# Kernel optimization log

Measured on AMD Instinct MI355X. Metric: run time of the kernel, lower is better.

Reference implementation:

```python
import jax, jax.numpy as jnp
import numpy as np

N_NODES = 50000
N_EDGES = 800000
D_IN = 128
D_H = 128
D_SIG = 16
D_OUT = 128


def _linear_params(key, fan_in, fan_out):
    kw, kb = jax.random.split(key)
    bound = 1.0 / np.sqrt(fan_in)
    w = jax.random.uniform(kw, (fan_in, fan_out), jnp.float32, -bound, bound)
    b = jax.random.uniform(kb, (fan_out,), jnp.float32, -bound, bound)
    return w, b


def setup_inputs() -> dict:
    key = jax.random.key(0)
    ks = jax.random.split(key, 7)
    x = jax.random.normal(ks[0], (N_NODES, D_IN), jnp.float32)
    edge_index = jax.random.randint(ks[1], (2, N_EDGES), 0, N_NODES, jnp.int64 if jax.config.jax_enable_x64 else jnp.int32)
    enc_w, enc_b = _linear_params(ks[2], D_IN, D_H)
    sig_w, sig_b = _linear_params(ks[3], D_H, D_SIG)
    msg_w, msg_b = _linear_params(ks[4], D_H, D_H)
    agg_w, agg_b = _linear_params(ks[5], 2 * D_H, D_H)
    dec_w, dec_b = _linear_params(ks[6], D_H, D_OUT)
    return {"x": x, "edge_index": edge_index,
            "enc_w": enc_w, "enc_b": enc_b,
            "sig_w": sig_w, "sig_b": sig_b,
            "msg_w": msg_w, "msg_b": msg_b,
            "agg_w": agg_w, "agg_b": agg_b,
            "dec_w": dec_w, "dec_b": dec_b}


def reference(x, edge_index, enc_w, enc_b, sig_w, sig_b, msg_w, msg_b, agg_w, agg_b, dec_w, dec_b):
    n = x.shape[0]
    h = x @ enc_w + enc_b                                   # [N, D_H]
    sig = h @ sig_w + sig_b                                 # [N, D_SIG]
    # F.normalize: x / max(||x||_2, eps)
    sig = sig / jnp.maximum(jnp.linalg.norm(sig, axis=-1, keepdims=True), 1e-12)
    msg = jax.nn.relu(h @ msg_w + msg_b)                    # [N, D_H]

    src, dst = edge_index[0], edge_index[1]
    # per-edge signature dot product, then segment softmax over each src node's edges
    scores = jnp.sum(sig[src] * sig[dst], axis=-1)          # [E]
    smax = jax.ops.segment_max(scores, src, num_segments=n)
    smax = jnp.where(jnp.isfinite(smax), smax, 0.0)         # empty segments -> 0
    e = jnp.exp(scores - smax[src])
    denom = jax.ops.segment_sum(e, src, num_segments=n)
    w = e / denom[src]                                      # [E]
    # weighted message aggregation; nodes with no out-edges get zeros
    comm = jax.ops.segment_sum(w[:, None] * msg[dst], src, num_segments=n)  # [N, D_H]

    combined = jax.nn.relu(jnp.concatenate([h, comm], axis=-1) @ agg_w + agg_b)
    return combined @ dec_w + dec_b
```

## Files before the change

kernel.cpp:

```cpp
#include <hip/hip_runtime.h>
#include <math.h>

#define N_NODES 50000
#define N_EDGES 800000
#define CAP 64
#define NRANGE 782
#define PCAP 1280
#define EPBA 8192
#define NBA 98

typedef __attribute__((ext_vector_type(8)))  short s16x8;
typedef __attribute__((ext_vector_type(16))) float f32x16;
typedef unsigned int u32;
typedef unsigned short u16;

union U16B { uint4 u; s16x8 s; };

__device__ __forceinline__ u32 bfr(float f) {
    u32 u = __float_as_uint(f);
    return (u + 0x7FFFu + ((u >> 16) & 1u)) >> 16;
}
__device__ __forceinline__ u32 pkbf(float a, float b) { return bfr(a) | (bfr(b) << 16); }
__device__ __forceinline__ float bf2f(u32 b) { return __uint_as_float(b << 16); }
__device__ __forceinline__ float dotpair(u32 a, u32 b) {
    return bf2f(a & 0xFFFFu) * bf2f(b & 0xFFFFu) + bf2f(a >> 16) * bf2f(b >> 16);
}

__device__ __forceinline__ uint4 buildfrag(const float* d8, int hh) {
    u32 P = pkbf(d8[0], d8[1]), Q = pkbf(d8[2], d8[3]);
    u32 R = pkbf(d8[4], d8[5]), S = pkbf(d8[6], d8[7]);
    u32 sP = (u32)__shfl_xor((int)P, 32);
    u32 sQ = (u32)__shfl_xor((int)Q, 32);
    u32 sR = (u32)__shfl_xor((int)R, 32);
    u32 sS = (u32)__shfl_xor((int)S, 32);
    uint4 f;
    f.x = hh ? sR : P;  f.y = hh ? sS : Q;
    f.z = hh ? R : sP;  f.w = hh ? S : sQ;
    return f;
}
#define BUILDF(OUT, ACC, Q, HH) do { \
    float _td[8]; \
    _Pragma("unroll") for (int _z = 0; _z < 8; ++_z) _td[_z] = (ACC)[(Q)*8 + _z]; \
    (OUT) = buildfrag(_td, HH); } while (0)
#define BUILDR(OUT, ACC, Q, HH) do { \
    float _td[8]; \
    _Pragma("unroll") for (int _z = 0; _z < 8; ++_z) _td[_z] = fmaxf((ACC)[(Q)*8 + _z], 0.f); \
    (OUT) = buildfrag(_td, HH); } while (0)

__global__ __launch_bounds__(256) void k_prep(
    const float* __restrict__ enc_w, const float* __restrict__ msg_w,
    const float* __restrict__ sig_w, const float* __restrict__ agg_w,
    const float* __restrict__ dec_w,
    uint4* __restrict__ WtE, uint4* __restrict__ WtM, uint4* __restrict__ WtD,
    uint4* __restrict__ WtA0, uint4* __restrict__ WtA1, uint4* __restrict__ WtS)
{
    int gid = blockIdx.x * 256 + threadIdx.x;
    if (gid < 10240) {
        int m = gid >> 11, r = gid & 2047;
        int col = r >> 4, s = r & 15;
        const float* W; uint4* D; int kb = 0;
        if      (m == 0) { W = enc_w; D = WtE; }
        else if (m == 1) { W = msg_w; D = WtM; }
        else if (m == 2) { W = dec_w; D = WtD; }
        else if (m == 3) { W = agg_w; D = WtA0; }
        else             { W = agg_w; D = WtA1; kb = 128; }
        float v[8];
        #pragma unroll
        for (int j = 0; j < 8; ++j) v[j] = W[(size_t)(kb + s * 8 + j) * 128 + col];
        uint4 w;
        w.x = pkbf(v[0], v[1]); w.y = pkbf(v[2], v[3]);
        w.z = pkbf(v[4], v[5]); w.w = pkbf(v[6], v[7]);
        D[col * 16 + (s ^ (col & 7))] = w;
    } else if (gid < 10752) {
        int r = gid - 10240;
        int row = r >> 4, s = r & 15;
        float v[8];
        #pragma unroll
        for (int j = 0; j < 8; ++j)
            v[j] = (row < 16) ? sig_w[(size_t)(s * 8 + j) * 16 + row] : 0.0f;
        uint4 w;
        w.x = pkbf(v[0], v[1]); w.y = pkbf(v[2], v[3]);
        w.z = pkbf(v[4], v[5]); w.w = pkbf(v[6], v[7]);
        WtS[row * 16 + (s ^ (row & 7))] = w;
    }
}

__global__ __launch_bounds__(256) void k_encode_m(
    const float* __restrict__ x,
    const uint4* __restrict__ WtE, const uint4* __restrict__ WtM,
    const uint4* __restrict__ WtS,
    const float* __restrict__ enc_b, const float* __restrict__ sig_b,
    const float* __restrict__ msg_b,
    uint4* __restrict__ h_g, u32* __restrict__ sig_bf, uint4* __restrict__ msg_g)
{
    __shared__ uint4 LB[2048];
    __shared__ uint4 LW[2048];
    __shared__ float LS[2176];

    const int t = threadIdx.x;
    const int node0 = blockIdx.x * 128;
    int nrem = N_NODES - node0; if (nrem > 128) nrem = 128;
    const int lane = t & 63, wid = t >> 6;
    const int l31 = lane & 31, hh = lane >> 5;
    const int nloc = wid * 32 + l31;
    const int sw7 = l31 & 7;

    #pragma unroll
    for (int it = 0; it < 8; ++it) {
        int idx = it * 256 + t;
        int nd = idx >> 4, s = idx & 15;
        float4 v0 = make_float4(0, 0, 0, 0), v1 = v0;
        if (nd < nrem) {
            const float4* px = (const float4*)(x + (size_t)(node0 + nd) * 128 + s * 8);
            v0 = px[0]; v1 = px[1];
        }
        uint4 w;
        w.x = pkbf(v0.x, v0.y); w.y = pkbf(v0.z, v0.w);
        w.z = pkbf(v1.x, v1.y); w.w = pkbf(v1.z, v1.w);
        LB[nd * 16 + (s ^ (nd & 7))] = w;
        LW[idx] = WtE[idx];
    }
    __syncthreads();

    const char* lb = (const char*)LB;
    const char* lw = (const char*)LW;

    f32x16 a0 = {}, a1 = {}, a2 = {}, a3 = {};
    #pragma unroll
    for (int r = 0; r < 16; ++r) {
        int rr = (r & 3) + 8 * (r >> 2) + 4 * hh;
        a0[r] = enc_b[rr];      a1[r] = enc_b[32 + rr];
        a2[r] = enc_b[64 + rr]; a3[r] = enc_b[96 + rr];
    }
    #pragma unroll
    for (int ks = 0; ks < 8; ++ks) {
        int so = ((ks * 2 + hh) ^ sw7) << 4;
        s16x8 bf = *(const s16x8*)(lb + nloc * 256 + so);
        s16x8 w0 = *(const s16x8*)(lw + l31 * 256 + so);
        s16x8 w1 = *(const s16x8*)(lw + 8192 + l31 * 256 + so);
        s16x8 w2 = *(const s16x8*)(lw + 16384 + l31 * 256 + so);
        s16x8 w3 = *(const s16x8*)(lw + 24576 + l31 * 256 + so);
        a0 = __builtin_amdgcn_mfma_f32_32x32x16_bf16(w0, bf, a0, 0, 0, 0);
        a1 = __builtin_amdgcn_mfma_f32_32x32x16_bf16(w1, bf, a1, 0, 0, 0);
        a2 = __builtin_amdgcn_mfma_f32_32x32x16_bf16(w2, bf, a2, 0, 0, 0);
        a3 = __builtin_amdgcn_mfma_f32_32x32x16_bf16(w3, bf, a3, 0, 0, 0);
    }

    uint4 hf[8];
    BUILDF(hf[0], a0, 0, hh); BUILDF(hf[1], a0, 1, hh);
    BUILDF(hf[2], a1, 0, hh); BUILDF(hf[3], a1, 1, hh);
    BUILDF(hf[4], a2, 0, hh); BUILDF(hf[5], a2, 1, hh);
    BUILDF(hf[6], a3, 0, hh); BUILDF(hf[7], a3, 1, hh);

    if (nloc < nrem) {
        const size_t rb = (size_t)(node0 + nloc) * 16;
        #pragma unroll
        for (int f = 0; f < 8; ++f) {
            int g = 2 * f + hh;
            h_g[rb + (g ^ sw7)] = hf[f];
        }
    }

    __syncthreads();
    #pragma unroll
    for (int it = 0; it < 8; ++it) LW[it * 256 + t] = WtM[it * 256 + t];
    {
        uint4* LSu = (uint4*)LS;
        LSu[t] = WtS[t]; LSu[256 + t] = WtS[256 + t];
    }
    __syncthreads();

    f32x16 m0 = {}, m1 = {}, m2 = {}, m3 = {};
    #pragma unroll
    for (int r = 0; r < 16; ++r) {
        int rr = (r & 3) + 8 * (r >> 2) + 4 * hh;
        m0[r] = msg_b[rr];      m1[r] = msg_b[32 + rr];
        m2[r] = msg_b[64 + rr]; m3[r] = msg_b[96 + rr];
    }
    #pragma unroll
    for (int ks = 0; ks < 8; ++ks) {
        int so = ((ks * 2 + hh) ^ sw7) << 4;
        U16B hb; hb.u = hf[ks];
        s16x8 w0 = *(const s16x8*)(lw + l31 * 256 + so);
        s16x8 w1 = *(const s16x8*)(lw + 8192 + l31 * 256 + so);
        s16x8 w2 = *(const s16x8*)(lw + 16384 + l31 * 256 + so);
        s16x8 w3 = *(const s16x8*)(lw + 24576 + l31 * 256 + so);
        m0 = __builtin_amdgcn_mfma_f32_32x32x16_bf16(w0, hb.s, m0, 0, 0, 0);
        m1 = __builtin_amdgcn_mfma_f32_32x32x16_bf16(w1, hb.s, m1, 0, 0, 0);
        m2 = __builtin_amdgcn_mfma_f32_32x32x16_bf16(w2, hb.s, m2, 0, 0, 0);
        m3 = __builtin_amdgcn_mfma_f32_32x32x16_bf16(w3, hb.s, m3, 0, 0, 0);
    }
    {
        uint4 mf[8];
        BUILDR(mf[0], m0, 0, hh); BUILDR(mf[1], m0, 1, hh);
        BUILDR(mf[2], m1, 0, hh); BUILDR(mf[3], m1, 1, hh);
        BUILDR(mf[4], m2, 0, hh); BUILDR(mf[5], m2, 1, hh);
        BUILDR(mf[6], m3, 0, hh); BUILDR(mf[7], m3, 1, hh);
        if (nloc < nrem) {
            const size_t rb = (size_t)(node0 + nloc) * 16;
            #pragma unroll
            for (int f = 0; f < 8; ++f) {
                int g = 2 * f + hh;
                msg_g[rb + g] = mf[f];
            }
        }
    }

    f32x16 sg = {};
    #pragma unroll
    for (int r = 0; r < 8; ++r) {
        int rr = (r & 3) + 8 * (r >> 2) + 4 * hh;
        sg[r] = sig_b[rr];
    }
    const char* lsw = (const char*)LS;
    #pragma unroll
    for (int ks = 0; ks < 8; ++ks) {
        int so = ((ks * 2 + hh) ^ sw7) << 4;
        s16x8 aw = *(const s16x8*)(lsw + l31 * 256 + so);
        U16B hb; hb.u = hf[ks];
        sg = __builtin_amdgcn_mfma_f32_32x32x16_bf16(aw, hb.s, sg, 0, 0, 0);
    }
    float ss = 0.f;
    #pragma unroll
    for (int r = 0; r < 8; ++r) ss += sg[r] * sg[r];
    ss += __shfl_xor(ss, 32);
    float inv = 1.0f / fmaxf(sqrtf(ss), 1e-12f);
    __syncthreads();
    #pragma unroll
    for (int r = 0; r < 8; ++r) {
        int sc = (r & 3) + 8 * (r >> 2) + 4 * hh;
        LS[nloc * 17 + sc] = sg[r] * inv;
    }
    __syncthreads();
    #pragma unroll
    for (int it = 0; it < 4; ++it) {
        int idx = it * 256 + t;
        int nd = idx >> 3, c2 = idx & 7;
        if (nd < nrem)
            sig_bf[(size_t)(node0 + nd) * 8 + c2] =
                pkbf(LS[nd * 17 + 2 * c2], LS[nd * 17 + 2 * c2 + 1]);
    }
}

__global__ __launch_bounds__(256) void k_decode_m(
    const uint4* __restrict__ h_g, const uint4* __restrict__ comm,
    const uint4* __restrict__ WtA0, const uint4* __restrict__ WtA1,
    const uint4* __restrict__ WtD,
    const float* __restrict__ agg_b, const float* __restrict__ dec_b,
    float* __restrict__ out)
{
    __shared__ uint4 LB[2048];
    __shared__ uint4 LW[2048];

    const int t = threadIdx.x;
    const int node0 = blockIdx.x * 64;
    int nrem = N_NODES - node0; if (nrem > 64) nrem = 64;
    const int lane = t & 63, wid = t >> 6;
    const int l31 = lane & 31, hh = lane >> 5;
    const int ng = wid & 1, cp = wid >> 1;
    const int nloc = ng * 32 + l31;
    const int sw7 = l31 & 7;

    #pragma unroll
    for (int it = 0; it < 8; ++it) {
        int idx = it * 256 + t;
        int nd = idx >> 5, g = idx & 31;
        uint4 v = make_uint4(0, 0, 0, 0);
        if (nd < nrem)
            v = (g < 16) ? h_g[(size_t)(node0 + nd) * 16 + g]
                         : comm[(size_t)(node0 + nd) * 16 + (g - 16)];
        LB[nd * 32 + g] = v;
        LW[idx] = WtA0[idx];
    }
    __syncthreads();

    const char* lb = (const char*)LB;
    const char* lw = (const char*)LW;

    f32x16 c0 = {}, c1 = {};
    #pragma unroll
    for (int r = 0; r < 16; ++r) {
        int rr = (r & 3) + 8 * (r >> 2) + 4 * hh;
        c0[r] = agg_b[cp * 64 + rr];
        c1[r] = agg_b[cp * 64 + 32 + rr];
    }
    #pragma unroll
    for (int ks = 0; ks < 8; ++ks) {
        int so = ((ks * 2 + hh) ^ sw7) << 4;
        s16x8 bf = *(const s16x8*)(lb + nloc * 512 + so);
        s16x8 w0 = *(const s16x8*)(lw + (cp * 64 + l31) * 256 + so);
        s16x8 w1 = *(const s16x8*)(lw + (cp * 64 + 32 + l31) * 256 + so);
        c0 = __builtin_amdgcn_mfma_f32_32x32x16_bf16(w0, bf, c0, 0, 0, 0);
        c1 = __builtin_amdgcn_mfma_f32_32x32x16_bf16(w1, bf, c1, 0, 0, 0);
    }
    __syncthreads();
    #pragma unroll
    for (int it = 0; it < 8; ++it) LW[it * 256 + t] = WtA1[it * 256 + t];
    __syncthreads();
    #pragma unroll
    for (int ks = 8; ks < 16; ++ks) {
        int so = ((ks * 2 + hh) ^ sw7) << 4;
        int so2 = (((ks - 8) * 2 + hh) ^ sw7) << 4;
        s16x8 bf = *(const s16x8*)(lb + nloc * 512 + so);
        s16x8 w0 = *(const s16x8*)(lw + (cp * 64 + l31) * 256 + so2);
        s16x8 w1 = *(const s16x8*)(lw + (cp * 64 + 32 + l31) * 256 + so2);
        c0 = __builtin_amdgcn_mfma_f32_32x32x16_bf16(w0, bf, c0, 0, 0, 0);
        c1 = __builtin_amdgcn_mfma_f32_32x32x16_bf16(w1, bf, c1, 0, 0, 0);
    }
    __syncthreads();

    {
        uint4 cf[4];
        BUILDR(cf[0], c0, 0, hh); BUILDR(cf[1], c0, 1, hh);
        BUILDR(cf[2], c1, 0, hh); BUILDR(cf[3], c1, 1, hh);
        #pragma unroll
        for (int f = 0; f < 4; ++f) {
            int g = (cp * 4 + f) * 2 + hh;
            LB[nloc * 16 + (g ^ sw7)] = cf[f];
        }
    }
    #pragma unroll
    for (int it = 0; it < 8; ++it) LW[it * 256 + t] = WtD[it * 256 + t];
    __syncthreads();

    f32x16 o0 = {}, o1 = {};
    {
        float b0 = dec_b[cp * 64 + l31], b1 = dec_b[cp * 64 + 32 + l31];
        #pragma unroll
        for (int r = 0; r < 16; ++r) { o0[r] = b0; o1[r] = b1; }
    }
    #pragma unroll
    for (int ks = 0; ks < 8; ++ks) {
        int so = ((ks * 2 + hh) ^ sw7) << 4;
        s16x8 af = *(const s16x8*)(lb + nloc * 256 + so);
        s16x8 w0 = *(const s16x8*)(lw + (cp * 64 + l31) * 256 + so);
        s16x8 w1 = *(const s16x8*)(lw + (cp * 64 + 32 + l31) * 256 + so);
        o0 = __builtin_amdgcn_mfma_f32_32x32x16_bf16(af, w0, o0, 0, 0, 0);
        o1 = __builtin_amdgcn_mfma_f32_32x32x16_bf16(af, w1, o1, 0, 0, 0);
    }
    #pragma unroll
    for (int r = 0; r < 16; ++r) {
        int nd = ng * 32 + (r & 3) + 8 * (r >> 2) + 4 * hh;
        if (nd < nrem) {
            float* row = out + (size_t)(node0 + nd) * 128 + cp * 64;
            row[l31]      = o0[r];
            row[32 + l31] = o1[r];
        }
    }
}

__global__ __launch_bounds__(256) void k_partA(
    const int* __restrict__ src, const int* __restrict__ dst,
    int* __restrict__ gcur, u32* __restrict__ part)
{
    __shared__ int hist[NRANGE];
    __shared__ int base[NRANGE];
    const int t = threadIdx.x;
    const int e0 = blockIdx.x * EPBA;

    for (int i = t; i < NRANGE; i += 256) hist[i] = 0;
    __syncthreads();
    #pragma unroll 4
    for (int k = 0; k < EPBA / 256; ++k) {
        int e = e0 + k * 256 + t;
        if (e < N_EDGES) atomicAdd(&hist[src[e] >> 6], 1);
    }
    __syncthreads();
    for (int i = t; i < NRANGE; i += 256) {
        int h = hist[i];
        base[i] = h ? atomicAdd(&gcur[i], h) : 0;
    }
    __syncthreads();
    for (int i = t; i < NRANGE; i += 256) hist[i] = 0;
    __syncthreads();
    #pragma unroll 4
    for (int k = 0; k < EPBA / 256; ++k) {
        int e = e0 + k * 256 + t;
        if (e < N_EDGES) {
            int s = src[e], d = dst[e];
            int r = s >> 6;
            int p = base[r] + atomicAdd(&hist[r], 1);
            part[(size_t)r * PCAP + p] = ((u32)s << 16) | (u32)d;
        }
    }
}

__global__ __launch_bounds__(256) void k_pb_aggr(
    const int* __restrict__ gcur, const u32* __restrict__ part,
    const u32* __restrict__ sig_bf,
    const char* __restrict__ msg_g, char* __restrict__ comm)
{
    __shared__ int   cnt[64];
    __shared__ float lden[64];
    __shared__ int2  lde[64 * CAP];

    const int t = threadIdx.x;
    const int r = blockIdx.x;
    const int node0 = r * 64;

    if (t < 64) { cnt[t] = 0; lden[t] = 0.f; }
    __syncthreads();

    const int total = gcur[r];
    for (int i = t; i < total; i += 256) {
        u32 en = part[(size_t)r * PCAP + i];
        int s = (int)(en >> 16), d = (int)(en & 0xFFFFu);
        const uint4* ps = (const uint4*)(sig_bf + (size_t)s * 8);
        const uint4* pd = (const uint4*)(sig_bf + (size_t)d * 8);
        uint4 sa = ps[0], sb = ps[1];
        uint4 da = pd[0], db = pd[1];
        float dot = dotpair(sa.x, da.x) + dotpair(sa.y, da.y)
                  + dotpair(sa.z, da.z) + dotpair(sa.w, da.w)
                  + dotpair(sb.x, db.x) + dotpair(sb.y, db.y)
                  + dotpair(sb.z, db.z) + dotpair(sb.w, db.w);
        float e = __expf(dot);
        int sl = s & 63;
        int p = atomicAdd(&cnt[sl], 1);
        lde[sl * CAP + p] = make_int2(d, __float_as_int(e));
        atomicAdd(&lden[sl], e);
    }
    __syncthreads();

    const int lane = t & 63, wid = t >> 6;
    const int l31 = lane & 31, hh = lane >> 5;
    #pragma unroll
    for (int g = 0; g < 8; ++g) {
        const int nloc = wid * 16 + 2 * g + hh;
        const int node = node0 + nloc;
        const int cn = cnt[nloc];
        float a0 = 0.f, a1 = 0.f, a2 = 0.f, a3 = 0.f;
        for (int k = 0; k < cn; ++k) {
            int2 de = lde[nloc * CAP + k];
            float e = __int_as_float(de.y);
            uint2 m = *(const uint2*)(msg_g + (size_t)de.x * 256 + 8 * l31);
            a0 += e * bf2f(m.x & 0xFFFFu);
            a1 += e * bf2f(m.x >> 16);
            a2 += e * bf2f(m.y & 0xFFFFu);
            a3 += e * bf2f(m.y >> 16);
        }
        float den = lden[nloc];
        float inv = (den > 0.f) ? (1.0f / den) : 0.f;
        if (node < N_NODES) {
            uint2 w;
            w.x = pkbf(a0 * inv, a1 * inv);
            w.y = pkbf(a2 * inv, a3 * inv);
            *(uint2*)(comm + (size_t)node * 256 + ((8 * l31) ^ ((node & 7) << 4))) = w;
        }
    }
}

extern "C" void kernel_launch(void* const* d_in, const int* in_sizes, int n_in,
                              void* d_out, int out_size, void* d_ws, size_t ws_size,
                              hipStream_t stream)
{
    const float* x     = (const float*)d_in[0];
    const int*   ei    = (const int*)  d_in[1];
    const float* enc_w = (const float*)d_in[2];
    const float* enc_b = (const float*)d_in[3];
    const float* sig_w = (const float*)d_in[4];
    const float* sig_b = (const float*)d_in[5];
    const float* msg_w = (const float*)d_in[6];
    const float* msg_b = (const float*)d_in[7];
    const float* agg_w = (const float*)d_in[8];
    const float* agg_b = (const float*)d_in[9];
    const float* dec_w = (const float*)d_in[10];
    const float* dec_b = (const float*)d_in[11];
    float* out = (float*)d_out;

    const int* src = ei;
    const int* dst = ei + N_EDGES;

    char* p = (char*)d_ws;
    uint4* h_g   = (uint4*)p;  p += (size_t)N_NODES * 256;
    uint4* msg_g = (uint4*)p;  p += (size_t)N_NODES * 256;
    uint4* comm  = (uint4*)p;  p += (size_t)N_NODES * 256;
    u32*   sig_bf = (u32*)p;   p += (size_t)N_NODES * 32;
    u32*   part   = (u32*)p;   p += (size_t)NRANGE * PCAP * 4;
    int*   gcur   = (int*)p;   p += 4096;
    uint4* WtE  = (uint4*)p; p += 32768;
    uint4* WtM  = (uint4*)p; p += 32768;
    uint4* WtD  = (uint4*)p; p += 32768;
    uint4* WtA0 = (uint4*)p; p += 32768;
    uint4* WtA1 = (uint4*)p; p += 32768;
    uint4* WtS  = (uint4*)p; p += 8192;

    hipMemsetAsync(gcur, 0, NRANGE * sizeof(int), stream);

    k_prep<<<42, 256, 0, stream>>>(enc_w, msg_w, sig_w, agg_w, dec_w,
                                   WtE, WtM, WtD, WtA0, WtA1, WtS);
    k_encode_m<<<(N_NODES + 127) / 128, 256, 0, stream>>>(
        x, WtE, WtM, WtS, enc_b, sig_b, msg_b, h_g, sig_bf, msg_g);
    k_partA<<<NBA, 256, 0, stream>>>(src, dst, gcur, part);
    k_pb_aggr<<<NRANGE, 256, 0, stream>>>(
        gcur, part, sig_bf, (const char*)msg_g, (char*)comm);
    k_decode_m<<<(N_NODES + 63) / 64, 256, 0, stream>>>(
        h_g, comm, WtA0, WtA1, WtD, agg_b, dec_b, out);
}
```

Measured before the change: 118.3 us.

## Fuse edge partitioning into encode launch and bucket edges by destination chunk

```diff
diff --git a/kernel.cpp b/kernel.cpp
--- a/kernel.cpp
+++ b/kernel.cpp
@@ -8,6 +8,8 @@
 #define PCAP 1280
 #define EPBA 8192
 #define NBA 98
+#define NBE 391
+#define NCHUNK 4
 
 typedef __attribute__((ext_vector_type(8)))  short s16x8;
 typedef __attribute__((ext_vector_type(16))) float f32x16;
@@ -52,9 +54,11 @@
     const float* __restrict__ sig_w, const float* __restrict__ agg_w,
     const float* __restrict__ dec_w,
     uint4* __restrict__ WtE, uint4* __restrict__ WtM, uint4* __restrict__ WtD,
-    uint4* __restrict__ WtA0, uint4* __restrict__ WtA1, uint4* __restrict__ WtS)
+    uint4* __restrict__ WtA0, uint4* __restrict__ WtA1, uint4* __restrict__ WtS,
+    int* __restrict__ gcur)
 {
     int gid = blockIdx.x * 256 + threadIdx.x;
+    if (gid < NRANGE) gcur[gid] = 0;
     if (gid < 10240) {
         int m = gid >> 11, r = gid & 2047;
         int col = r >> 4, s = r & 15;
@@ -85,19 +89,54 @@
     }
 }
 
-__global__ __launch_bounds__(256) void k_encode_m(
+__global__ __launch_bounds__(256) void k_enc_part(
     const float* __restrict__ x,
     const uint4* __restrict__ WtE, const uint4* __restrict__ WtM,
     const uint4* __restrict__ WtS,
     const float* __restrict__ enc_b, const float* __restrict__ sig_b,
     const float* __restrict__ msg_b,
-    uint4* __restrict__ h_g, u32* __restrict__ sig_bf, uint4* __restrict__ msg_g)
+    uint4* __restrict__ h_g, u32* __restrict__ sig_bf, uint4* __restrict__ msg_g,
+    const int* __restrict__ src, const int* __restrict__ dst,
+    int* __restrict__ gcur, u32* __restrict__ part)
 {
     __shared__ uint4 LB[2048];
     __shared__ uint4 LW[2048];
     __shared__ float LS[2176];
 
     const int t = threadIdx.x;
+
+    if (blockIdx.x >= NBE) {
+        int* hist = (int*)LB;
+        int* base = hist + NRANGE;
+        const int e0 = (blockIdx.x - NBE) * EPBA;
+        for (int i = t; i < NRANGE; i += 256) hist[i] = 0;
+        __syncthreads();
+        #pragma unroll 4
+        for (int k = 0; k < EPBA / 256; ++k) {
+            int e = e0 + k * 256 + t;
+            if (e < N_EDGES) atomicAdd(&hist[src[e] >> 6], 1);
+        }
+        __syncthreads();
+        for (int i = t; i < NRANGE; i += 256) {
+            int h = hist[i];
+            base[i] = h ? atomicAdd(&gcur[i], h) : 0;
+        }
+        __syncthreads();
+        for (int i = t; i < NRANGE; i += 256) hist[i] = 0;
+        __syncthreads();
+        #pragma unroll 4
+        for (int k = 0; k < EPBA / 256; ++k) {
+            int e = e0 + k * 256 + t;
+            if (e < N_EDGES) {
+                int s = src[e], d = dst[e];
+                int r = s >> 6;
+                int p = base[r] + atomicAdd(&hist[r], 1);
+                part[(size_t)r * PCAP + p] = ((u32)s << 16) | (u32)d;
+            }
+        }
+        return;
+    }
+
     const int node0 = blockIdx.x * 128;
     int nrem = N_NODES - node0; if (nrem > 128) nrem = 128;
     const int lane = t & 63, wid = t >> 6;
@@ -349,48 +388,13 @@
     }
 }
 
-__global__ __launch_bounds__(256) void k_partA(
-    const int* __restrict__ src, const int* __restrict__ dst,
-    int* __restrict__ gcur, u32* __restrict__ part)
-{
-    __shared__ int hist[NRANGE];
-    __shared__ int base[NRANGE];
-    const int t = threadIdx.x;
-    const int e0 = blockIdx.x * EPBA;
-
-    for (int i = t; i < NRANGE; i += 256) hist[i] = 0;
-    __syncthreads();
-    #pragma unroll 4
-    for (int k = 0; k < EPBA / 256; ++k) {
-        int e = e0 + k * 256 + t;
-        if (e < N_EDGES) atomicAdd(&hist[src[e] >> 6], 1);
-    }
-    __syncthreads();
-    for (int i = t; i < NRANGE; i += 256) {
-        int h = hist[i];
-        base[i] = h ? atomicAdd(&gcur[i], h) : 0;
-    }
-    __syncthreads();
-    for (int i = t; i < NRANGE; i += 256) hist[i] = 0;
-    __syncthreads();
-    #pragma unroll 4
-    for (int k = 0; k < EPBA / 256; ++k) {
-        int e = e0 + k * 256 + t;
-        if (e < N_EDGES) {
-            int s = src[e], d = dst[e];
-            int r = s >> 6;
-            int p = base[r] + atomicAdd(&hist[r], 1);
-            part[(size_t)r * PCAP + p] = ((u32)s << 16) | (u32)d;
-        }
-    }
-}
-
 __global__ __launch_bounds__(256) void k_pb_aggr(
     const int* __restrict__ gcur, const u32* __restrict__ part,
     const u32* __restrict__ sig_bf,
     const char* __restrict__ msg_g, char* __restrict__ comm)
 {
-    __shared__ int   cnt[64];
+    __shared__ int   cnt4[64 * NCHUNK];
+    __shared__ int   ctot[64];
     __shared__ float lden[64];
     __shared__ int2  lde[64 * CAP];
 
@@ -398,10 +402,29 @@
     const int r = blockIdx.x;
     const int node0 = r * 64;
 
-    if (t < 64) { cnt[t] = 0; lden[t] = 0.f; }
+    for (int i = t; i < 64 * NCHUNK; i += 256) cnt4[i] = 0;
+    if (t < 64) lden[t] = 0.f;
     __syncthreads();
 
     const int total = gcur[r];
+    for (int i = t; i < total; i += 256) {
+        u32 en = part[(size_t)r * PCAP + i];
+        int sl = (int)((en >> 16) & 63);
+        int c  = (int)((en & 0xFFFFu) / 12500u);
+        atomicAdd(&cnt4[sl * NCHUNK + c], 1);
+    }
+    __syncthreads();
+    if (t < 64) {
+        int b = 0;
+        #pragma unroll
+        for (int c = 0; c < NCHUNK; ++c) {
+            int v = cnt4[t * NCHUNK + c];
+            cnt4[t * NCHUNK + c] = b;
+            b += v;
+        }
+        ctot[t] = b;
+    }
+    __syncthreads();
     for (int i = t; i < total; i += 256) {
         u32 en = part[(size_t)r * PCAP + i];
         int s = (int)(en >> 16), d = (int)(en & 0xFFFFu);
@@ -415,7 +438,8 @@
                   + dotpair(sb.z, db.z) + dotpair(sb.w, db.w);
         float e = __expf(dot);
         int sl = s & 63;
-        int p = atomicAdd(&cnt[sl], 1);
+        int c  = d / 12500;
+        int p  = atomicAdd(&cnt4[sl * NCHUNK + c], 1);
         lde[sl * CAP + p] = make_int2(d, __float_as_int(e));
         atomicAdd(&lden[sl], e);
     }
@@ -427,7 +451,7 @@
     for (int g = 0; g < 8; ++g) {
         const int nloc = wid * 16 + 2 * g + hh;
         const int node = node0 + nloc;
-        const int cn = cnt[nloc];
+        const int cn = ctot[nloc];
         float a0 = 0.f, a1 = 0.f, a2 = 0.f, a3 = 0.f;
         for (int k = 0; k < cn; ++k) {
             int2 de = lde[nloc * CAP + k];
@@ -484,13 +508,11 @@
     uint4* WtA1 = (uint4*)p; p += 32768;
     uint4* WtS  = (uint4*)p; p += 8192;
 
-    hipMemsetAsync(gcur, 0, NRANGE * sizeof(int), stream);
-
     k_prep<<<42, 256, 0, stream>>>(enc_w, msg_w, sig_w, agg_w, dec_w,
-                                   WtE, WtM, WtD, WtA0, WtA1, WtS);
-    k_encode_m<<<(N_NODES + 127) / 128, 256, 0, stream>>>(
-        x, WtE, WtM, WtS, enc_b, sig_b, msg_b, h_g, sig_bf, msg_g);
-    k_partA<<<NBA, 256, 0, stream>>>(src, dst, gcur, part);
+                                   WtE, WtM, WtD, WtA0, WtA1, WtS, gcur);
+    k_enc_part<<<NBE + NBA, 256, 0, stream>>>(
+        x, WtE, WtM, WtS, enc_b, sig_b, msg_b, h_g, sig_bf, msg_g,
+        src, dst, gcur, part);
     k_pb_aggr<<<NRANGE, 256, 0, stream>>>(
         gcur, part, sig_bf, (const char*)msg_g, (char*)comm);
     k_decode_m<<<(N_NODES + 63) / 64, 256, 0, stream>>>(
```

After: 101.8 us. -14.0%, faster.

## Fuse edge partitioning into encode kernel, read weights from global, unroll gather

Applied to the files above, without the earlier changes.

```diff
diff --git a/kernel.cpp b/kernel.cpp
--- a/kernel.cpp
+++ b/kernel.cpp
@@ -6,8 +6,9 @@
 #define CAP 64
 #define NRANGE 782
 #define PCAP 1280
-#define EPBA 8192
-#define NBA 98
+#define EPBA 2560
+#define NBA 313
+#define NBE 391
 
 typedef __attribute__((ext_vector_type(8)))  short s16x8;
 typedef __attribute__((ext_vector_type(16))) float f32x16;
@@ -52,9 +53,11 @@
     const float* __restrict__ sig_w, const float* __restrict__ agg_w,
     const float* __restrict__ dec_w,
     uint4* __restrict__ WtE, uint4* __restrict__ WtM, uint4* __restrict__ WtD,
-    uint4* __restrict__ WtA0, uint4* __restrict__ WtA1, uint4* __restrict__ WtS)
+    uint4* __restrict__ WtA0, uint4* __restrict__ WtA1, uint4* __restrict__ WtS,
+    int* __restrict__ gcur)
 {
     int gid = blockIdx.x * 256 + threadIdx.x;
+    if (gid < NRANGE) gcur[gid] = 0;
     if (gid < 10240) {
         int m = gid >> 11, r = gid & 2047;
         int col = r >> 4, s = r & 15;
@@ -85,19 +88,53 @@
     }
 }
 
-__global__ __launch_bounds__(256) void k_encode_m(
+__global__ __launch_bounds__(256) void k_enc_part(
     const float* __restrict__ x,
     const uint4* __restrict__ WtE, const uint4* __restrict__ WtM,
     const uint4* __restrict__ WtS,
     const float* __restrict__ enc_b, const float* __restrict__ sig_b,
     const float* __restrict__ msg_b,
-    uint4* __restrict__ h_g, u32* __restrict__ sig_bf, uint4* __restrict__ msg_g)
+    uint4* __restrict__ h_g, u32* __restrict__ sig_bf, uint4* __restrict__ msg_g,
+    const int* __restrict__ src, const int* __restrict__ dst,
+    int* __restrict__ gcur, u32* __restrict__ part)
 {
     __shared__ uint4 LB[2048];
-    __shared__ uint4 LW[2048];
     __shared__ float LS[2176];
 
     const int t = threadIdx.x;
+
+    if (blockIdx.x >= NBE) {
+        int* hist = (int*)LB;
+        int* base = hist + NRANGE;
+        const int e0 = (blockIdx.x - NBE) * EPBA;
+        for (int i = t; i < NRANGE; i += 256) hist[i] = 0;
+        __syncthreads();
+        #pragma unroll 4
+        for (int k = 0; k < EPBA / 256; ++k) {
+            int e = e0 + k * 256 + t;
+            if (e < N_EDGES) atomicAdd(&hist[src[e] >> 6], 1);
+        }
+        __syncthreads();
+        for (int i = t; i < NRANGE; i += 256) {
+            int h = hist[i];
+            base[i] = h ? atomicAdd(&gcur[i], h) : 0;
+        }
+        __syncthreads();
+        for (int i = t; i < NRANGE; i += 256) hist[i] = 0;
+        __syncthreads();
+        #pragma unroll 4
+        for (int k = 0; k < EPBA / 256; ++k) {
+            int e = e0 + k * 256 + t;
+            if (e < N_EDGES) {
+                int s = src[e], d = dst[e];
+                int r = s >> 6;
+                int p = base[r] + atomicAdd(&hist[r], 1);
+                part[(size_t)r * PCAP + p] = ((u32)s << 16) | (u32)d;
+            }
+        }
+        return;
+    }
+
     const int node0 = blockIdx.x * 128;
     int nrem = N_NODES - node0; if (nrem > 128) nrem = 128;
     const int lane = t & 63, wid = t >> 6;
@@ -118,12 +155,13 @@
         w.x = pkbf(v0.x, v0.y); w.y = pkbf(v0.z, v0.w);
         w.z = pkbf(v1.x, v1.y); w.w = pkbf(v1.z, v1.w);
         LB[nd * 16 + (s ^ (nd & 7))] = w;
-        LW[idx] = WtE[idx];
     }
     __syncthreads();
 
     const char* lb = (const char*)LB;
-    const char* lw = (const char*)LW;
+    const char* gwE = (const char*)WtE;
+    const char* gwM = (const char*)WtM;
+    const char* gwS = (const char*)WtS;
 
     f32x16 a0 = {}, a1 = {}, a2 = {}, a3 = {};
     #pragma unroll
@@ -136,10 +174,10 @@
     for (int ks = 0; ks < 8; ++ks) {
         int so = ((ks * 2 + hh) ^ sw7) << 4;
         s16x8 bf = *(const s16x8*)(lb + nloc * 256 + so);
-        s16x8 w0 = *(const s16x8*)(lw + l31 * 256 + so);
-        s16x8 w1 = *(const s16x8*)(lw + 8192 + l31 * 256 + so);
-        s16x8 w2 = *(const s16x8*)(lw + 16384 + l31 * 256 + so);
-        s16x8 w3 = *(const s16x8*)(lw + 24576 + l31 * 256 + so);
+        s16x8 w0 = *(const s16x8*)(gwE + l31 * 256 + so);
+        s16x8 w1 = *(const s16x8*)(gwE + 8192 + l31 * 256 + so);
+        s16x8 w2 = *(const s16x8*)(gwE + 16384 + l31 * 256 + so);
+        s16x8 w3 = *(const s16x8*)(gwE + 24576 + l31 * 256 + so);
         a0 = __builtin_amdgcn_mfma_f32_32x32x16_bf16(w0, bf, a0, 0, 0, 0);
         a1 = __builtin_amdgcn_mfma_f32_32x32x16_bf16(w1, bf, a1, 0, 0, 0);
         a2 = __builtin_amdgcn_mfma_f32_32x32x16_bf16(w2, bf, a2, 0, 0, 0);
@@ -161,15 +199,6 @@
         }
     }
 
-    __syncthreads();
-    #pragma unroll
-    for (int it = 0; it < 8; ++it) LW[it * 256 + t] = WtM[it * 256 + t];
-    {
-        uint4* LSu = (uint4*)LS;
-        LSu[t] = WtS[t]; LSu[256 + t] = WtS[256 + t];
-    }
-    __syncthreads();
-
     f32x16 m0 = {}, m1 = {}, m2 = {}, m3 = {};
     #pragma unroll
     for (int r = 0; r < 16; ++r) {
@@ -181,10 +210,10 @@
     for (int ks = 0; ks < 8; ++ks) {
         int so = ((ks * 2 + hh) ^ sw7) << 4;
         U16B hb; hb.u = hf[ks];
-        s16x8 w0 = *(const s16x8*)(lw + l31 * 256 + so);
-        s16x8 w1 = *(const s16x8*)(lw + 8192 + l31 * 256 + so);
-        s16x8 w2 = *(const s16x8*)(lw + 16384 + l31 * 256 + so);
-        s16x8 w3 = *(const s16x8*)(lw + 24576 + l31 * 256 + so);
+        s16x8 w0 = *(const s16x8*)(gwM + l31 * 256 + so);
+        s16x8 w1 = *(const s16x8*)(gwM + 8192 + l31 * 256 + so);
+        s16x8 w2 = *(const s16x8*)(gwM + 16384 + l31 * 256 + so);
+        s16x8 w3 = *(const s16x8*)(gwM + 24576 + l31 * 256 + so);
         m0 = __builtin_amdgcn_mfma_f32_32x32x16_bf16(w0, hb.s, m0, 0, 0, 0);
         m1 = __builtin_amdgcn_mfma_f32_32x32x16_bf16(w1, hb.s, m1, 0, 0, 0);
         m2 = __builtin_amdgcn_mfma_f32_32x32x16_bf16(w2, hb.s, m2, 0, 0, 0);
@@ -212,11 +241,10 @@
         int rr = (r & 3) + 8 * (r >> 2) + 4 * hh;
         sg[r] = sig_b[rr];
     }
-    const char* lsw = (const char*)LS;
     #pragma unroll
     for (int ks = 0; ks < 8; ++ks) {
         int so = ((ks * 2 + hh) ^ sw7) << 4;
-        s16x8 aw = *(const s16x8*)(lsw + l31 * 256 + so);
+        s16x8 aw = *(const s16x8*)(gwS + l31 * 256 + so);
         U16B hb; hb.u = hf[ks];
         sg = __builtin_amdgcn_mfma_f32_32x32x16_bf16(aw, hb.s, sg, 0, 0, 0);
     }
@@ -225,7 +253,6 @@
     for (int r = 0; r < 8; ++r) ss += sg[r] * sg[r];
     ss += __shfl_xor(ss, 32);
     float inv = 1.0f / fmaxf(sqrtf(ss), 1e-12f);
-    __syncthreads();
     #pragma unroll
     for (int r = 0; r < 8; ++r) {
         int sc = (r & 3) + 8 * (r >> 2) + 4 * hh;
@@ -345,42 +372,6 @@
             float* row = out + (size_t)(node0 + nd) * 128 + cp * 64;
             row[l31]      = o0[r];
             row[32 + l31] = o1[r];
-        }
-    }
-}
-
-__global__ __launch_bounds__(256) void k_partA(
-    const int* __restrict__ src, const int* __restrict__ dst,
-    int* __restrict__ gcur, u32* __restrict__ part)
-{
-    __shared__ int hist[NRANGE];
-    __shared__ int base[NRANGE];
-    const int t = threadIdx.x;
-    const int e0 = blockIdx.x * EPBA;
-
-    for (int i = t; i < NRANGE; i += 256) hist[i] = 0;
-    __syncthreads();
-    #pragma unroll 4
-    for (int k = 0; k < EPBA / 256; ++k) {
-        int e = e0 + k * 256 + t;
-        if (e < N_EDGES) atomicAdd(&hist[src[e] >> 6], 1);
-    }
-    __syncthreads();
-    for (int i = t; i < NRANGE; i += 256) {
-        int h = hist[i];
-        base[i] = h ? atomicAdd(&gcur[i], h) : 0;
-    }
-    __syncthreads();
-    for (int i = t; i < NRANGE; i += 256) hist[i] = 0;
-    __syncthreads();
-    #pragma unroll 4
-    for (int k = 0; k < EPBA / 256; ++k) {
-        int e = e0 + k * 256 + t;
-        if (e < N_EDGES) {
-            int s = src[e], d = dst[e];
-            int r = s >> 6;
-            int p = base[r] + atomicAdd(&hist[r], 1);
-            part[(size_t)r * PCAP + p] = ((u32)s << 16) | (u32)d;
         }
     }
 }
@@ -428,9 +419,28 @@
         const int nloc = wid * 16 + 2 * g + hh;
         const int node = node0 + nloc;
         const int cn = cnt[nloc];
+        const int2* ld = &lde[nloc * CAP];
         float a0 = 0.f, a1 = 0.f, a2 = 0.f, a3 = 0.f;
-        for (int k = 0; k < cn; ++k) {
-            int2 de = lde[nloc * CAP + k];
+        int k = 0;
+        for (; k + 4 <= cn; k += 4) {
+            int2 d0 = ld[k], d1 = ld[k + 1], d2 = ld[k + 2], d3 = ld[k + 3];
+            uint2 m0 = *(const uint2*)(msg_g + (size_t)d0.x * 256 + 8 * l31);
+            uint2 m1 = *(const uint2*)(msg_g + (size_t)d1.x * 256 + 8 * l31);
+            uint2 m2 = *(const uint2*)(msg_g + (size_t)d2.x * 256 + 8 * l31);
+            uint2 m3 = *(const uint2*)(msg_g + (size_t)d3.x * 256 + 8 * l31);
+            float e0 = __int_as_float(d0.y), e1 = __int_as_float(d1.y);
+            float e2 = __int_as_float(d2.y), e3 = __int_as_float(d3.y);
+            a0 += e0 * bf2f(m0.x & 0xFFFFu); a1 += e0 * bf2f(m0.x >> 16);
+            a2 += e0 * bf2f(m0.y & 0xFFFFu); a3 += e0 * bf2f(m0.y >> 16);
+            a0 += e1 * bf2f(m1.x & 0xFFFFu); a1 += e1 * bf2f(m1.x >> 16);
+            a2 += e1 * bf2f(m1.y & 0xFFFFu); a3 += e1 * bf2f(m1.y >> 16);
+            a0 += e2 * bf2f(m2.x & 0xFFFFu); a1 += e2 * bf2f(m2.x >> 16);
+            a2 += e2 * bf2f(m2.y & 0xFFFFu); a3 += e2 * bf2f(m2.y >> 16);
+            a0 += e3 * bf2f(m3.x & 0xFFFFu); a1 += e3 * bf2f(m3.x >> 16);
+            a2 += e3 * bf2f(m3.y & 0xFFFFu); a3 += e3 * bf2f(m3.y >> 16);
+        }
+        for (; k < cn; ++k) {
+            int2 de = ld[k];
             float e = __int_as_float(de.y);
             uint2 m = *(const uint2*)(msg_g + (size_t)de.x * 256 + 8 * l31);
             a0 += e * bf2f(m.x & 0xFFFFu);
@@ -484,13 +494,11 @@
     uint4* WtA1 = (uint4*)p; p += 32768;
     uint4* WtS  = (uint4*)p; p += 8192;
 
-    hipMemsetAsync(gcur, 0, NRANGE * sizeof(int), stream);
-
     k_prep<<<42, 256, 0, stream>>>(enc_w, msg_w, sig_w, agg_w, dec_w,
-                                   WtE, WtM, WtD, WtA0, WtA1, WtS);
-    k_encode_m<<<(N_NODES + 127) / 128, 256, 0, stream>>>(
-        x, WtE, WtM, WtS, enc_b, sig_b, msg_b, h_g, sig_bf, msg_g);
-    k_partA<<<NBA, 256, 0, stream>>>(src, dst, gcur, part);
+                                   WtE, WtM, WtD, WtA0, WtA1, WtS, gcur);
+    k_enc_part<<<NBE + NBA, 256, 0, stream>>>(
+        x, WtE, WtM, WtS, enc_b, sig_b, msg_b, h_g, sig_bf, msg_g,
+        src, dst, gcur, part);
     k_pb_aggr<<<NRANGE, 256, 0, stream>>>(
         gcur, part, sig_bf, (const char*)msg_g, (char*)comm);
     k_decode_m<<<(N_NODES + 63) / 64, 256, 0, stream>>>(
```

Result: faster. 95.79 us (-19.0%).
